# Kernel optimization log

Measured on AMD Instinct MI355X. Metric: run time of the kernel, lower is better.

Reference implementation:

```python
import jax, jax.numpy as jnp
import numpy as np

DIM = 2048
HQ = 32
HKV = 8
HEAD_DIM = DIM // HQ          # 64
GROUP = HQ // HKV             # 4 q-heads per kv-head
B, S = 2, 2048


def setup_inputs() -> dict:
    key = jax.random.key(0)
    ks = jax.random.split(key, 12)
    sc_in = 1.0 / np.sqrt(DIM)   # lecun_normal fan-in scaling
    inp = {
        "q": jax.random.normal(ks[0], (B, S, DIM), jnp.float32),
        "k": jax.random.normal(ks[1], (B, S, DIM), jnp.float32),
        "v": jax.random.normal(ks[2], (B, S, DIM), jnp.float32),
        # causal 0/1 mask: module computes scores -= 1/mask + 1, so 0 -> -inf (masked), 1 -> -2 (softmax-invariant shift)
        "mask": jnp.tril(jnp.ones((S, S), jnp.int32)),
        "Wq": jax.random.normal(ks[3], (DIM, HQ * HEAD_DIM), jnp.float32) * sc_in,
        "bq": jnp.zeros((HQ * HEAD_DIM,), jnp.float32),
        "Wk": jax.random.normal(ks[4], (DIM, HKV * HEAD_DIM), jnp.float32) * sc_in,
        "bk": jnp.zeros((HKV * HEAD_DIM,), jnp.float32),
        "Wv": jax.random.normal(ks[5], (DIM, HKV * HEAD_DIM), jnp.float32) * sc_in,
        "bv": jnp.zeros((HKV * HEAD_DIM,), jnp.float32),
        "Wo": jax.random.normal(ks[6], (DIM, DIM), jnp.float32) * (1.0 / np.sqrt(DIM)),
        "bo": jnp.zeros((DIM,), jnp.float32),
    }
    return inp


def reference(q, k, v, mask, Wq, bq, Wk, bk, Wv, bv, Wo, bo):
    b, s, _ = q.shape
    # projections -> per-head layout
    qx = (q @ Wq + bq).reshape(b, s, HKV, GROUP, HEAD_DIM)   # grouped q-heads
    kx = (k @ Wk + bk).reshape(b, s, HKV, HEAD_DIM)
    vx = (v @ Wv + bv).reshape(b, s, HKV, HEAD_DIM)
    # scores[b, h, g, i, j] = q_i . k_j ; same math as repeating kv heads GROUP times
    scores = jnp.einsum('bihgd,bjhd->bhgij', qx, kx) / jnp.sqrt(
        jnp.asarray(HEAD_DIM, qx.dtype))
    # module's masking: scores -= 1/mask + 1  (mask==0 -> -inf, mask==1 -> -2)
    scores = scores - (1.0 / mask.astype(scores.dtype) + 1.0)
    probs = jax.nn.softmax(scores, axis=-1)
    out = jnp.einsum('bhgij,bjhd->bihgd', probs, vx).reshape(b, s, DIM)
    out = out @ Wo + bo
    return out
```

## Files before the change

kernel.cpp:

```cpp
#include <hip/hip_runtime.h>

typedef unsigned short u16;
typedef unsigned int u32;
typedef __attribute__((ext_vector_type(8))) short short8v;
typedef __attribute__((ext_vector_type(4))) float f32x4;

#define DIM 2048
#define HQN 32
#define HKVN 8
#define HD 64
#define BB 2
#define SS 2048
#define MTOT (BB*SS)
#define NKV (HKVN*HD)

__device__ __forceinline__ u16 f2bf(float f){
  u32 u = __float_as_uint(f);
  u += 0x7FFFu + ((u >> 16) & 1u);
  return (u16)(u >> 16);
}

__device__ __forceinline__ u32 cvtpk(float a, float b){
  u32 r; asm("v_cvt_pk_bf16_f32 %0, %1, %2" : "=v"(r) : "v"(a), "v"(b)); return r;
}

__device__ __forceinline__ void gload_lds16(const void* g, void* l){
  __builtin_amdgcn_global_load_lds((const __attribute__((address_space(1))) u32*)g,
                                   (__attribute__((address_space(3))) u32*)l, 16, 0, 0);
}

#define WAITVM_(N) asm volatile("s_waitcnt vmcnt(" #N ")" ::: "memory")
#define WAITVM(N) WAITVM_(N)
#define CFENCE()  asm volatile("" ::: "memory")
#define BARF()    do { CFENCE(); __builtin_amdgcn_s_barrier(); CFENCE(); } while(0)
#define MF(a,b,cc) __builtin_amdgcn_mfma_f32_16x16x32_bf16((a),(b),(cc),0,0,0)

__global__ __launch_bounds__(256) void cast3_kernel(const float4* __restrict__ q,
                                                    const float4* __restrict__ k,
                                                    const float4* __restrict__ v,
                                                    u16* __restrict__ qo,
                                                    u16* __restrict__ ko,
                                                    u16* __restrict__ vo, int n4){
  const int z = blockIdx.y;
  const float4* in = z==0 ? q : (z==1 ? k : v);
  u16* out = z==0 ? qo : (z==1 ? ko : vo);
  int i = blockIdx.x*256 + threadIdx.x;
  if (i < n4){
    float4 f = in[i];
    union { u16 s[4]; unsigned long long u; } r;
    r.s[0]=f2bf(f.x); r.s[1]=f2bf(f.y); r.s[2]=f2bf(f.z); r.s[3]=f2bf(f.w);
    *(unsigned long long*)(out + (size_t)i*4) = r.u;
  }
}

__global__ __launch_bounds__(256) void transpose4_kernel(const float* __restrict__ Wq,
                                                         const float* __restrict__ Wk,
                                                         const float* __restrict__ Wv,
                                                         const float* __restrict__ Wo,
                                                         u16* __restrict__ WqT,
                                                         u16* __restrict__ WkT,
                                                         u16* __restrict__ WvT,
                                                         u16* __restrict__ WoT){
  const int z = blockIdx.z;
  const float* W = z==0?Wq:(z==1?Wk:(z==2?Wv:Wo));
  u16* WT = z==0?WqT:(z==1?WkT:(z==2?WvT:WoT));
  const int N = (z==1||z==2) ? NKV : DIM;
  const int K = DIM;
  int n0 = blockIdx.x*32, k0 = blockIdx.y*32;
  if (n0 >= N) return;
  __shared__ float tile[32][33];
  int tx = threadIdx.x & 31, ty = threadIdx.x >> 5;
  #pragma unroll
  for (int i=0;i<4;i++){
    int kk = ty + i*8;
    tile[kk][tx] = W[(size_t)(k0+kk)*N + n0 + tx];
  }
  __syncthreads();
  #pragma unroll
  for (int i=0;i<4;i++){
    int n = ty + i*8;
    WT[(size_t)(n0+n)*K + k0 + tx] = f2bf(tile[tx][n]);
  }
}

template<int MODE>
__global__ __launch_bounds__(512, 4) void gemm_pipe_kernel(
    const u16* __restrict__ Aq, const u16* __restrict__ Ak, const u16* __restrict__ Av,
    const u16* __restrict__ BT,
    const float* __restrict__ bq, const float* __restrict__ bk, const float* __restrict__ bv,
    u16* __restrict__ Qp, u16* __restrict__ Kp, u16* __restrict__ Vp,
    float* __restrict__ Cout)
{
  __shared__ __align__(16) u16 lds[3][12288];
  const int t = threadIdx.x, lane = t & 63, w = t >> 6;
  const int wm = w >> 1, wn = w & 1, g = lane >> 4, c = lane & 15;
  int bid = blockIdx.x;
  int seg, m0, n0;
  if (MODE == 0){
    bid = (bid & 7)*48 + (bid >> 3);
    if (bid < 256){ seg = 0; m0 = (bid >> 4)*256; n0 = (bid & 15)*128; }
    else { int u = bid - 256; seg = 1 + (u >> 6); int u6 = u & 63;
           m0 = (u6 >> 2)*256; n0 = (seg == 1 ? 2048 : 2560) + (u6 & 3)*128; }
  } else {
    bid = (bid & 7)*32 + (bid >> 3);
    seg = 0; m0 = (bid >> 4)*256; n0 = (bid & 15)*128;
  }
  const u16* A = (MODE==1 || seg==0) ? Aq : (seg==1 ? Ak : Av);
  const float* bias = (MODE==1 || seg==0) ? bq : (seg==1 ? bk : bv);
  const int nsegbase = (MODE==1 || seg==0) ? 0 : (seg==1 ? 2048 : 2560);

  const u16* gA0 = A  + (size_t)(m0 +       (t>>2))*DIM + (t&3)*8;
  const u16* gA1 = A  + (size_t)(m0 + 128 + (t>>2))*DIM + (t&3)*8;
  const u16* gB  = BT + (size_t)(n0 +       (t>>2))*DIM + (t&3)*8;

#define STG_A(KT, SL) do{ size_t ko_=(size_t)(KT)*32; \
    gload_lds16(gA0+ko_, &lds[SL][t*8]); \
    gload_lds16(gA1+ko_, &lds[SL][4096 + t*8]); }while(0)
#define STG_B(KT, SL) do{ \
    gload_lds16(gB + (size_t)(KT)*32, &lds[SL][8192 + t*8]); }while(0)

  const f32x4 fzero = {0.f,0.f,0.f,0.f};
  f32x4 acc[4][4];
  #pragma unroll
  for (int i=0;i<4;i++)
    #pragma unroll
    for (int j=0;j<4;j++) acc[i][j] = fzero;

  const int arow = wm*64 + c;
  const int brow = wn*64 + c;

#define TILE(SC, SG, KT, DOSTAGE, DOVM, VMN) do{                                \
    const u16* Ls_ = &lds[SC][0];                                               \
    short8v a0_ = *(const short8v*)&Ls_[(arow +  0)*32 + 8*g];                  \
    short8v a1_ = *(const short8v*)&Ls_[(arow + 16)*32 + 8*g];                  \
    short8v b0_ = *(const short8v*)&Ls_[8192 + (brow +  0)*32 + 8*g];           \
    short8v b1_ = *(const short8v*)&Ls_[8192 + (brow + 16)*32 + 8*g];           \
    short8v b2_ = *(const short8v*)&Ls_[8192 + (brow + 32)*32 + 8*g];           \
    short8v b3_ = *(const short8v*)&Ls_[8192 + (brow + 48)*32 + 8*g];           \
    if (DOSTAGE) STG_A((KT)+2, SG);                                             \
    BARF();                                                                     \
    __builtin_amdgcn_s_setprio(1);                                              \
    acc[0][0]=MF(a0_,b0_,acc[0][0]); acc[0][1]=MF(a0_,b1_,acc[0][1]);           \
    acc[0][2]=MF(a0_,b2_,acc[0][2]); acc[0][3]=MF(a0_,b3_,acc[0][3]);           \
    acc[1][0]=MF(a1_,b0_,acc[1][0]); acc[1][1]=MF(a1_,b1_,acc[1][1]);           \
    acc[1][2]=MF(a1_,b2_,acc[1][2]); acc[1][3]=MF(a1_,b3_,acc[1][3]);           \
    __builtin_amdgcn_s_setprio(0);                                              \
    BARF();                                                                     \
    short8v a2_ = *(const short8v*)&Ls_[(arow + 32)*32 + 8*g];                  \
    short8v a3_ = *(const short8v*)&Ls_[(arow + 48)*32 + 8*g];                  \
    if (DOSTAGE) STG_B((KT)+2, SG);                                             \
    BARF();                                                                     \
    __builtin_amdgcn_s_setprio(1);                                              \
    acc[2][0]=MF(a2_,b0_,acc[2][0]); acc[2][1]=MF(a2_,b1_,acc[2][1]);           \
    acc[2][2]=MF(a2_,b2_,acc[2][2]); acc[2][3]=MF(a2_,b3_,acc[2][3]);           \
    acc[3][0]=MF(a3_,b0_,acc[3][0]); acc[3][1]=MF(a3_,b1_,acc[3][1]);           \
    acc[3][2]=MF(a3_,b2_,acc[3][2]); acc[3][3]=MF(a3_,b3_,acc[3][3]);           \
    __builtin_amdgcn_s_setprio(0);                                              \
    if (DOVM) WAITVM(VMN);                                                      \
    BARF();                                                                     \
  }while(0)

  STG_A(0, 0); STG_B(0, 0);
  STG_A(1, 1); STG_B(1, 1);
  WAITVM(3);
  BARF();

  for (int tt = 0; tt < 62; ++tt){
    const int sc = tt % 3;
    const int sg = (tt + 2) % 3;
    TILE(sc, sg, tt, 1, 1, 3);
  }
  TILE(62 % 3, 0, 62, 0, 1, 0);
  TILE(63 % 3, 0, 63, 0, 0, 0);
#undef TILE
#undef STG_A
#undef STG_B

  __syncthreads();

  if (MODE == 1){
    #pragma unroll
    for (int fm=0; fm<4; fm++){
      #pragma unroll
      for (int fn=0; fn<4; fn++){
        int n = n0 + wn*64 + fn*16 + c;
        float bvv = bias[n];
        #pragma unroll
        for (int r=0; r<4; r++){
          int m = m0 + wm*64 + fm*16 + 4*g + r;
          Cout[(size_t)m*DIM + n] = acc[fm][fn][r] + bvv;
        }
      }
    }
  } else {
    u16* st = &lds[0][0] + w*4096;
    if (seg == 2){
      #pragma unroll
      for (int fm=0; fm<4; fm++){
        #pragma unroll
        for (int fn=0; fn<4; fn++){
          float bvv = bias[n0 - nsegbase + wn*64 + fn*16 + c];
          int vbase = (fm>>1)*2048 + fn*512 + (g*16 + c)*8 + (fm&1)*4;
          *(u32*)&st[vbase]     = cvtpk(acc[fm][fn][0]+bvv, acc[fm][fn][1]+bvv);
          *(u32*)&st[vbase + 2] = cvtpk(acc[fm][fn][2]+bvv, acc[fm][fn][3]+bvv);
        }
      }
    } else {
      #pragma unroll
      for (int fm=0; fm<4; fm++){
        #pragma unroll
        for (int fn=0; fn<4; fn++){
          float bvv = bias[n0 - nsegbase + wn*64 + fn*16 + c];
          int sbase = (fm>>1)*2048 + ((fm&1)*2 + (fn>>1))*512
                    + (c>>2)*128 + (fn&1)*4 + (c&3);
          #pragma unroll
          for (int r=0; r<4; r++)
            st[sbase + (4*g + r)*8] = f2bf(acc[fm][fn][r] + bvv);
        }
      }
    }
    __syncthreads();
    const int bb = m0 >> 11;
    const int st0 = ((m0 & 2047) >> 5) + wm*2;
    u16* dst;
    if (seg == 0)      dst = Qp + (((size_t)bb*HQN  + (n0>>6)        + wn) << 17);
    else if (seg == 1) dst = Kp + (((size_t)bb*HKVN + ((n0-2048)>>6) + wn) << 17);
    else               dst = Vp + (((size_t)bb*HKVN + ((n0-2560)>>6) + wn) << 17);
    dst += (size_t)st0*2048;
    #pragma unroll
    for (int i=0;i<8;i++)
      *(short8v*)(dst + lane*8 + i*512) = *(const short8v*)(st + lane*8 + i*512);
  }
}

__global__ __launch_bounds__(256) void attn_kernel(const u16* __restrict__ Qp,
                                                   const u16* __restrict__ Kp,
                                                   const u16* __restrict__ Vp,
                                                   u16* __restrict__ Aout){
  const int grp = blockIdx.x & 15;
  const int jj  = blockIdx.x >> 4;
  const int b   = grp >> 3;
  const int hkv = grp & 7;
  const int t = threadIdx.x;
  const int lane = t & 63, w = t >> 6;
  const int g = lane >> 4, c = lane & 15;
  const int hq = hkv*4 + w;

  __shared__ __align__(16) u16 Kt[2][2048];
  __shared__ __align__(16) u16 Vt[2][2048];

  const u16* Kb = Kp + (((size_t)b*HKVN + hkv) << 17);
  const u16* Vb = Vp + (((size_t)b*HKVN + hkv) << 17);
  const u16* Qb = Qp + (((size_t)b*HQN + hq) << 17);
  const float SCL = 0.18033688011112042f;
  const f32x4 fzero = {0.f,0.f,0.f,0.f};

  for (int half = 0; half < 2; ++half){
    const int T = half ? jj : (63 - jj);

    short8v qf[2][2];
    {
      const u16* qs = Qb + (size_t)T*2048 + lane*8;
      qf[0][0] = *(const short8v*)(qs);
      qf[0][1] = *(const short8v*)(qs + 512);
      qf[1][0] = *(const short8v*)(qs + 1024);
      qf[1][1] = *(const short8v*)(qs + 1536);
    }
    float l_r[2] = {0.f, 0.f};
    f32x4 o[2][4];
    #pragma unroll
    for (int qi=0; qi<2; qi++)
      #pragma unroll
      for (int f=0; f<4; f++) o[qi][f] = fzero;

    gload_lds16(Kb + t*8, &Kt[0][t*8]);
    gload_lds16(Vb + t*8, &Vt[0][t*8]);
    asm volatile("s_waitcnt vmcnt(0)" ::: "memory");
    __syncthreads();

    int cur = 0;
    for (int kt = 0; kt <= T; ++kt){
      if (kt < T){
        gload_lds16(Kb + (size_t)(kt+1)*2048 + t*8, &Kt[cur^1][t*8]);
        gload_lds16(Vb + (size_t)(kt+1)*2048 + t*8, &Vt[cur^1][t*8]);
      }
      short8v kf0 = *(const short8v*)&Kt[cur][lane*8];
      short8v kf1 = *(const short8v*)&Kt[cur][512 + lane*8];
      short8v kf2 = *(const short8v*)&Kt[cur][1024 + lane*8];
      short8v kf3 = *(const short8v*)&Kt[cur][1536 + lane*8];
      short8v vf0 = *(const short8v*)&Vt[cur][lane*8];
      short8v vf1 = *(const short8v*)&Vt[cur][512 + lane*8];
      short8v vf2 = *(const short8v*)&Vt[cur][1024 + lane*8];
      short8v vf3 = *(const short8v*)&Vt[cur][1536 + lane*8];
      const bool diag = (kt == T);
      #pragma unroll
      for (int qi=0; qi<2; qi++){
        f32x4 s0 = fzero, s1 = fzero;
        __builtin_amdgcn_s_setprio(1);
        s0 = MF(kf0, qf[qi][0], s0);
        s0 = MF(kf1, qf[qi][1], s0);
        s1 = MF(kf2, qf[qi][0], s1);
        s1 = MF(kf3, qf[qi][1], s1);
        __builtin_amdgcn_s_setprio(0);
        float p0[4], p1[4];
        #pragma unroll
        for (int r=0; r<4; r++){
          p0[r] = __builtin_amdgcn_exp2f(s0[r]*SCL);
          p1[r] = __builtin_amdgcn_exp2f(s1[r]*SCL);
        }
        if (diag){
          const int qloc = qi*16 + c;
          #pragma unroll
          for (int r=0; r<4; r++){
            if (4*g + r      > qloc) p0[r] = 0.f;
            if (16 + 4*g + r > qloc) p1[r] = 0.f;
          }
        }
        l_r[qi] += (p0[0]+p0[1]) + (p0[2]+p0[3]) + (p1[0]+p1[1]) + (p1[2]+p1[3]);
        union { u32 u[4]; short8v v; } pu;
        pu.u[0] = cvtpk(p0[0], p0[1]);
        pu.u[1] = cvtpk(p0[2], p0[3]);
        pu.u[2] = cvtpk(p1[0], p1[1]);
        pu.u[3] = cvtpk(p1[2], p1[3]);
        __builtin_amdgcn_s_setprio(1);
        o[qi][0] = MF(pu.v, vf0, o[qi][0]);
        o[qi][1] = MF(pu.v, vf1, o[qi][1]);
        o[qi][2] = MF(pu.v, vf2, o[qi][2]);
        o[qi][3] = MF(pu.v, vf3, o[qi][3]);
        __builtin_amdgcn_s_setprio(0);
      }
      asm volatile("s_waitcnt vmcnt(0)" ::: "memory");
      __syncthreads();
      cur ^= 1;
    }

    #pragma unroll
    for (int qi=0; qi<2; qi++){
      float ls = l_r[qi];
      ls += __shfl_xor(ls, 16);
      ls += __shfl_xor(ls, 32);
      float li = 1.0f / ls;
      float lf[4];
      #pragma unroll
      for (int r=0; r<4; r++) lf[r] = __shfl(li, 4*g + r);
      #pragma unroll
      for (int f=0; f<4; f++){
        #pragma unroll
        for (int r=0; r<4; r++){
          int q = T*32 + qi*16 + 4*g + r;
          Aout[((size_t)b*SS + q)*DIM + hq*HD + f*16 + c] = f2bf(o[qi][f][r]*lf[r]);
        }
      }
    }
  }
}

extern "C" void kernel_launch(void* const* d_in, const int* in_sizes, int n_in,
                              void* d_out, int out_size, void* d_ws, size_t ws_size,
                              hipStream_t stream){
  const float* q  = (const float*)d_in[0];
  const float* k  = (const float*)d_in[1];
  const float* v  = (const float*)d_in[2];
  const float* Wq = (const float*)d_in[4];
  const float* bq = (const float*)d_in[5];
  const float* Wk = (const float*)d_in[6];
  const float* bk = (const float*)d_in[7];
  const float* Wv = (const float*)d_in[8];
  const float* bv = (const float*)d_in[9];
  const float* Wo = (const float*)d_in[10];
  const float* bo = (const float*)d_in[11];
  float* out = (float*)d_out;

  char* ws = (char*)d_ws;
  u16* q_bf = (u16*)ws; ws += (size_t)MTOT*DIM*2;
  u16* k_bf = (u16*)ws; ws += (size_t)MTOT*DIM*2;
  u16* v_bf = (u16*)ws; ws += (size_t)MTOT*DIM*2;
  u16* WqT  = (u16*)ws; ws += (size_t)DIM*DIM*2;
  u16* WkT  = (u16*)ws; ws += (size_t)NKV*DIM*2;
  u16* WvT  = (u16*)ws; ws += (size_t)NKV*DIM*2;
  u16* WoT  = (u16*)ws; ws += (size_t)DIM*DIM*2;
  u16* Qp   = (u16*)ws; ws += (size_t)MTOT*DIM*2;
  u16* Kp   = (u16*)ws; ws += (size_t)MTOT*NKV*2;
  u16* Vp   = (u16*)ws; ws += (size_t)MTOT*NKV*2;
  u16* attn = (u16*)ws; ws += (size_t)MTOT*DIM*2;

  const int n4 = MTOT*DIM/4;
  cast3_kernel<<<dim3(n4/256, 3), 256, 0, stream>>>((const float4*)q, (const float4*)k,
                                                    (const float4*)v, q_bf, k_bf, v_bf, n4);
  transpose4_kernel<<<dim3(DIM/32, DIM/32, 4), 256, 0, stream>>>(Wq, Wk, Wv, Wo,
                                                                 WqT, WkT, WvT, WoT);
  gemm_pipe_kernel<0><<<384, 512, 0, stream>>>(q_bf, k_bf, v_bf, WqT,
                                               bq, bk, bv, Qp, Kp, Vp, nullptr);
  attn_kernel<<<512, 256, 0, stream>>>(Qp, Kp, Vp, attn);
  gemm_pipe_kernel<1><<<256, 512, 0, stream>>>(attn, nullptr, nullptr, WoT,
                                               bo, nullptr, nullptr,
                                               nullptr, nullptr, nullptr, out);
}
```

Before: 216.3 us.

## Split GEMM into larger-tile QKV and O kernels with swizzled double-buffered LDS

Replaces the shared templated GEMM with two specialised kernels. The QKV projection moves to 256x256 tiles (192 blocks, 8x4 accumulators per warp), and the output GEMM keeps 256x128 tiles but uses a 2x4 warp grid. Both now use K=64 steps with XOR-swizzled LDS and a double-buffered, four-phase load/compute schedule. The aim is more data reuse per byte loaded and fewer LDS bank conflicts. The cost is much more LDS and more registers per block, which lowers occupancy (launch bounds drop to 2 blocks per CU), and the QKV launch has fewer blocks than the machine has CUs, which can hurt wave balance.

```diff
diff --git a/kernel.cpp b/kernel.cpp
--- a/kernel.cpp
+++ b/kernel.cpp
@@ -83,154 +83,265 @@
   }
 }
 
-template<int MODE>
-__global__ __launch_bounds__(512, 4) void gemm_pipe_kernel(
-    const u16* __restrict__ Aq, const u16* __restrict__ Ak, const u16* __restrict__ Av,
-    const u16* __restrict__ BT,
-    const float* __restrict__ bq, const float* __restrict__ bk, const float* __restrict__ bv,
-    u16* __restrict__ Qp, u16* __restrict__ Kp, u16* __restrict__ Vp,
-    float* __restrict__ Cout)
-{
-  __shared__ __align__(16) u16 lds[3][12288];
+__global__ __launch_bounds__(512, 2) void gemm_qkv_kernel(const u16* __restrict__ Aq,
+                                                          const u16* __restrict__ Ak,
+                                                          const u16* __restrict__ Av,
+                                                          const u16* __restrict__ BT,
+                                                          const float* __restrict__ bq,
+                                                          const float* __restrict__ bk,
+                                                          const float* __restrict__ bv,
+                                                          u16* __restrict__ Qp,
+                                                          u16* __restrict__ Kp,
+                                                          u16* __restrict__ Vp){
+  __shared__ __align__(16) u16 lds[65536];
+  char* ldsb = (char*)lds;
   const int t = threadIdx.x, lane = t & 63, w = t >> 6;
-  const int wm = w >> 1, wn = w & 1, g = lane >> 4, c = lane & 15;
+  const int wm = w >> 2, wn = w & 3, g = lane >> 4, c = lane & 15;
   int bid = blockIdx.x;
-  int seg, m0, n0;
-  if (MODE == 0){
-    bid = (bid & 7)*48 + (bid >> 3);
-    if (bid < 256){ seg = 0; m0 = (bid >> 4)*256; n0 = (bid & 15)*128; }
-    else { int u = bid - 256; seg = 1 + (u >> 6); int u6 = u & 63;
-           m0 = (u6 >> 2)*256; n0 = (seg == 1 ? 2048 : 2560) + (u6 & 3)*128; }
-  } else {
-    bid = (bid & 7)*32 + (bid >> 3);
-    seg = 0; m0 = (bid >> 4)*256; n0 = (bid & 15)*128;
-  }
-  const u16* A = (MODE==1 || seg==0) ? Aq : (seg==1 ? Ak : Av);
-  const float* bias = (MODE==1 || seg==0) ? bq : (seg==1 ? bk : bv);
-  const int nsegbase = (MODE==1 || seg==0) ? 0 : (seg==1 ? 2048 : 2560);
-
-  const u16* gA0 = A  + (size_t)(m0 +       (t>>2))*DIM + (t&3)*8;
-  const u16* gA1 = A  + (size_t)(m0 + 128 + (t>>2))*DIM + (t&3)*8;
-  const u16* gB  = BT + (size_t)(n0 +       (t>>2))*DIM + (t&3)*8;
-
-#define STG_A(KT, SL) do{ size_t ko_=(size_t)(KT)*32; \
-    gload_lds16(gA0+ko_, &lds[SL][t*8]); \
-    gload_lds16(gA1+ko_, &lds[SL][4096 + t*8]); }while(0)
-#define STG_B(KT, SL) do{ \
-    gload_lds16(gB + (size_t)(KT)*32, &lds[SL][8192 + t*8]); }while(0)
+  bid = (bid & 7)*24 + (bid >> 3);
+  const int mt = bid / 12, nt = bid - mt*12;
+  const int m0 = mt*256, n0 = nt*256;
+  const int seg = (n0 >= 2560) ? 2 : (n0 >= 2048 ? 1 : 0);
+  const u16* A = seg==0 ? Aq : (seg==1 ? Ak : Av);
+  const float* bias = seg==0 ? bq : (seg==1 ? bk : bv);
+  const int nbase = seg==0 ? 0 : (seg==1 ? 2048 : 2560);
+
+  const int rA = t >> 3;
+  const int kc = ((t & 7) ^ (rA & 7)) * 8;
+  const u16* gA = A  + (size_t)(m0 + rA)*DIM + kc;
+  const u16* gB = BT + (size_t)(n0 + ((rA>>5)<<6) + (rA & 31))*DIM + kc;
+
+  const u32 ko0 = (u32)((g*16) ^ ((c&7)<<4));
+  const u32 ko1 = (u32)((64 + g*16) ^ ((c&7)<<4));
+  const u32 aoff = wm*8192 + c*128;
+  const u32 boff = wn*4096 + c*128;
+
+#define STGA_(PA, KT, ABASE) do{ \
+    gload_lds16(gA + (size_t)(KT)*64 + (size_t)((PA)*64)*DIM,       ldsb + (ABASE) + (PA)*16384 + t*16); \
+    gload_lds16(gA + (size_t)(KT)*64 + (size_t)((PA)*64+128)*DIM,   ldsb + (ABASE) + (PA)*16384 + 8192 + t*16); }while(0)
+#define STGB_(PB, KT, BBASE) do{ \
+    gload_lds16(gB + (size_t)(KT)*64 + (size_t)((PB)*32)*DIM,       ldsb + (BBASE) + (PB)*16384 + t*16); \
+    gload_lds16(gB + (size_t)(KT)*64 + (size_t)((PB)*32+128)*DIM,   ldsb + (BBASE) + (PB)*16384 + 8192 + t*16); }while(0)
+#define LD8(OFF) (*(const short8v*)(ldsb + (OFF)))
 
   const f32x4 fzero = {0.f,0.f,0.f,0.f};
-  f32x4 acc[4][4];
+  f32x4 acc[8][4];
   #pragma unroll
-  for (int i=0;i<4;i++)
+  for (int i=0;i<8;i++)
     #pragma unroll
     for (int j=0;j<4;j++) acc[i][j] = fzero;
 
-  const int arow = wm*64 + c;
-  const int brow = wn*64 + c;
-
-#define TILE(SC, SG, KT, DOSTAGE, DOVM, VMN) do{                                \
-    const u16* Ls_ = &lds[SC][0];                                               \
-    short8v a0_ = *(const short8v*)&Ls_[(arow +  0)*32 + 8*g];                  \
-    short8v a1_ = *(const short8v*)&Ls_[(arow + 16)*32 + 8*g];                  \
-    short8v b0_ = *(const short8v*)&Ls_[8192 + (brow +  0)*32 + 8*g];           \
-    short8v b1_ = *(const short8v*)&Ls_[8192 + (brow + 16)*32 + 8*g];           \
-    short8v b2_ = *(const short8v*)&Ls_[8192 + (brow + 32)*32 + 8*g];           \
-    short8v b3_ = *(const short8v*)&Ls_[8192 + (brow + 48)*32 + 8*g];           \
-    if (DOSTAGE) STG_A((KT)+2, SG);                                             \
-    BARF();                                                                     \
-    __builtin_amdgcn_s_setprio(1);                                              \
-    acc[0][0]=MF(a0_,b0_,acc[0][0]); acc[0][1]=MF(a0_,b1_,acc[0][1]);           \
-    acc[0][2]=MF(a0_,b2_,acc[0][2]); acc[0][3]=MF(a0_,b3_,acc[0][3]);           \
-    acc[1][0]=MF(a1_,b0_,acc[1][0]); acc[1][1]=MF(a1_,b1_,acc[1][1]);           \
-    acc[1][2]=MF(a1_,b2_,acc[1][2]); acc[1][3]=MF(a1_,b3_,acc[1][3]);           \
-    __builtin_amdgcn_s_setprio(0);                                              \
-    BARF();                                                                     \
-    short8v a2_ = *(const short8v*)&Ls_[(arow + 32)*32 + 8*g];                  \
-    short8v a3_ = *(const short8v*)&Ls_[(arow + 48)*32 + 8*g];                  \
-    if (DOSTAGE) STG_B((KT)+2, SG);                                             \
-    BARF();                                                                     \
-    __builtin_amdgcn_s_setprio(1);                                              \
-    acc[2][0]=MF(a2_,b0_,acc[2][0]); acc[2][1]=MF(a2_,b1_,acc[2][1]);           \
-    acc[2][2]=MF(a2_,b2_,acc[2][2]); acc[2][3]=MF(a2_,b3_,acc[2][3]);           \
-    acc[3][0]=MF(a3_,b0_,acc[3][0]); acc[3][1]=MF(a3_,b1_,acc[3][1]);           \
-    acc[3][2]=MF(a3_,b2_,acc[3][2]); acc[3][3]=MF(a3_,b3_,acc[3][3]);           \
-    __builtin_amdgcn_s_setprio(0);                                              \
-    if (DOVM) WAITVM(VMN);                                                      \
-    BARF();                                                                     \
+#define MM16(FM0, FN0) do{ __builtin_amdgcn_s_setprio(1); \
+    _Pragma("unroll") for (int q=0;q<4;q++) \
+      _Pragma("unroll") for (int s=0;s<2;s++){ \
+        acc[(FM0)+q][(FN0)+s] = MF(a_[q][0], b_[s][0], acc[(FM0)+q][(FN0)+s]); \
+        acc[(FM0)+q][(FN0)+s] = MF(a_[q][1], b_[s][1], acc[(FM0)+q][(FN0)+s]); } \
+    __builtin_amdgcn_s_setprio(0); }while(0)
+
+#define RD_A(PABASE) do{ _Pragma("unroll") for (int q=0;q<4;q++){ \
+    a_[q][0] = LD8((PABASE) + aoff + q*2048 + ko0); \
+    a_[q][1] = LD8((PABASE) + aoff + q*2048 + ko1); } }while(0)
+#define RD_B(PBBASE) do{ _Pragma("unroll") for (int q=0;q<2;q++){ \
+    b_[q][0] = LD8((PBBASE) + boff + q*2048 + ko0); \
+    b_[q][1] = LD8((PBBASE) + boff + q*2048 + ko1); } }while(0)
+
+#define QSTEP(TT, CUR, DOSTG, TAIL) do{ \
+    const u32 AC = (CUR)*32768,  BC = 65536 + (CUR)*32768; \
+    const u32 AN = (CUR^1)*32768, BN = 65536 + (CUR^1)*32768; \
+    short8v a_[4][2], b_[2][2]; \
+    RD_A(AC); RD_B(BC); \
+    if (DOSTG) STGA_(0, (TT)+1, AN); \
+    BARF(); \
+    MM16(0,0); \
+    if (TAIL) { WAITVM(2); } else { WAITVM(4); } \
+    BARF(); \
+    RD_B(BC + 16384); \
+    if (DOSTG) STGB_(0, (TT)+1, BN); \
+    BARF(); \
+    MM16(0,2); \
+    if (TAIL) { WAITVM(0); } else { WAITVM(4); } \
+    BARF(); \
+    RD_A(AC + 16384); \
+    if (DOSTG) STGB_(1, (TT)+1, BN); \
+    BARF(); \
+    MM16(4,2); \
+    BARF(); \
+    RD_B(BC); \
+    if (DOSTG) STGA_(1, (TT)+1, AN); \
+    BARF(); \
+    MM16(4,0); \
+    if (!TAIL) { WAITVM(4); } \
+    BARF(); \
   }while(0)
 
-  STG_A(0, 0); STG_B(0, 0);
-  STG_A(1, 1); STG_B(1, 1);
-  WAITVM(3);
+  STGA_(0, 0, 0); STGB_(0, 0, 65536); STGB_(1, 0, 65536); STGA_(1, 0, 0);
+  WAITVM(0);
   BARF();
 
-  for (int tt = 0; tt < 62; ++tt){
-    const int sc = tt % 3;
-    const int sg = (tt + 2) % 3;
-    TILE(sc, sg, tt, 1, 1, 3);
-  }
-  TILE(62 % 3, 0, 62, 0, 1, 0);
-  TILE(63 % 3, 0, 63, 0, 0, 0);
-#undef TILE
-#undef STG_A
-#undef STG_B
-
+  #pragma unroll 1
+  for (int tt = 0; tt < 30; tt += 2){
+    QSTEP(tt,   0, 1, 0);
+    QSTEP(tt+1, 1, 1, 0);
+  }
+  QSTEP(30, 0, 1, 0);
+  QSTEP(31, 1, 0, 1);
+#undef QSTEP
+
+  WAITVM(0);
   __syncthreads();
 
-  if (MODE == 1){
-    #pragma unroll
-    for (int fm=0; fm<4; fm++){
+  u16* st = lds + w*8192;
+  if (seg == 2){
+    #pragma unroll
+    for (int fm=0; fm<8; fm++){
       #pragma unroll
       for (int fn=0; fn<4; fn++){
-        int n = n0 + wn*64 + fn*16 + c;
-        float bvv = bias[n];
-        #pragma unroll
-        for (int r=0; r<4; r++){
-          int m = m0 + wm*64 + fm*16 + 4*g + r;
-          Cout[(size_t)m*DIM + n] = acc[fm][fn][r] + bvv;
-        }
+        float bvv = bias[n0 - nbase + wn*64 + fn*16 + c];
+        int vbase = (fm>>1)*2048 + fn*512 + (g*16 + c)*8 + (fm&1)*4;
+        *(u32*)&st[vbase]     = cvtpk(acc[fm][fn][0]+bvv, acc[fm][fn][1]+bvv);
+        *(u32*)&st[vbase + 2] = cvtpk(acc[fm][fn][2]+bvv, acc[fm][fn][3]+bvv);
       }
     }
   } else {
-    u16* st = &lds[0][0] + w*4096;
-    if (seg == 2){
-      #pragma unroll
-      for (int fm=0; fm<4; fm++){
+    #pragma unroll
+    for (int fm=0; fm<8; fm++){
+      #pragma unroll
+      for (int fn=0; fn<4; fn++){
+        float bvv = bias[n0 - nbase + wn*64 + fn*16 + c];
+        int sbase = (fm>>1)*2048 + ((fm&1)*2 + (fn>>1))*512 + (c>>2)*128 + (fn&1)*4 + (c&3);
         #pragma unroll
-        for (int fn=0; fn<4; fn++){
-          float bvv = bias[n0 - nsegbase + wn*64 + fn*16 + c];
-          int vbase = (fm>>1)*2048 + fn*512 + (g*16 + c)*8 + (fm&1)*4;
-          *(u32*)&st[vbase]     = cvtpk(acc[fm][fn][0]+bvv, acc[fm][fn][1]+bvv);
-          *(u32*)&st[vbase + 2] = cvtpk(acc[fm][fn][2]+bvv, acc[fm][fn][3]+bvv);
-        }
-      }
-    } else {
-      #pragma unroll
-      for (int fm=0; fm<4; fm++){
-        #pragma unroll
-        for (int fn=0; fn<4; fn++){
-          float bvv = bias[n0 - nsegbase + wn*64 + fn*16 + c];
-          int sbase = (fm>>1)*2048 + ((fm&1)*2 + (fn>>1))*512
-                    + (c>>2)*128 + (fn&1)*4 + (c&3);
-          #pragma unroll
-          for (int r=0; r<4; r++)
-            st[sbase + (4*g + r)*8] = f2bf(acc[fm][fn][r] + bvv);
-        }
+        for (int r=0; r<4; r++)
+          st[sbase + (4*g + r)*8] = f2bf(acc[fm][fn][r] + bvv);
       }
     }
-    __syncthreads();
+  }
+  __syncthreads();
+  {
     const int bb = m0 >> 11;
-    const int st0 = ((m0 & 2047) >> 5) + wm*2;
+    const int st0 = ((m0 & 2047) >> 5) + wm*4;
     u16* dst;
     if (seg == 0)      dst = Qp + (((size_t)bb*HQN  + (n0>>6)        + wn) << 17);
     else if (seg == 1) dst = Kp + (((size_t)bb*HKVN + ((n0-2048)>>6) + wn) << 17);
     else               dst = Vp + (((size_t)bb*HKVN + ((n0-2560)>>6) + wn) << 17);
     dst += (size_t)st0*2048;
     #pragma unroll
-    for (int i=0;i<8;i++)
+    for (int i=0;i<16;i++)
       *(short8v*)(dst + lane*8 + i*512) = *(const short8v*)(st + lane*8 + i*512);
   }
+#undef STGA_
+#undef STGB_
+#undef RD_A
+#undef RD_B
+#undef MM16
+}
+
+__global__ __launch_bounds__(512, 2) void gemm_o_kernel(const u16* __restrict__ A,
+                                                        const u16* __restrict__ BT,
+                                                        const float* __restrict__ bias,
+                                                        float* __restrict__ C){
+  __shared__ __align__(16) u16 lds[49152];
+  char* ldsb = (char*)lds;
+  const int t = threadIdx.x, lane = t & 63, w = t >> 6;
+  const int wm = w >> 2, wn = w & 3, g = lane >> 4, c = lane & 15;
+  int bid = blockIdx.x;
+  bid = (bid & 7)*32 + (bid >> 3);
+  const int m0 = (bid >> 4)*256, n0 = (bid & 15)*128;
+
+  const int rA = t >> 3;
+  const int kc = ((t & 7) ^ (rA & 7)) * 8;
+  const u16* gA = A  + (size_t)(m0 + rA)*DIM + kc;
+  const u16* gB = BT + (size_t)(n0 + ((rA>>4)<<5) + (rA & 15))*DIM + kc;
+
+  const u32 ko0 = (u32)((g*16) ^ ((c&7)<<4));
+  const u32 ko1 = (u32)((64 + g*16) ^ ((c&7)<<4));
+  const u32 aoff = wm*8192 + c*128;
+  const u32 boffo = wn*2048 + c*128;
+
+#define STGA_(PA, KT, ABASE) do{ \
+    gload_lds16(gA + (size_t)(KT)*64 + (size_t)((PA)*64)*DIM,       ldsb + (ABASE) + (PA)*16384 + t*16); \
+    gload_lds16(gA + (size_t)(KT)*64 + (size_t)((PA)*64+128)*DIM,   ldsb + (ABASE) + (PA)*16384 + 8192 + t*16); }while(0)
+#define STGB_(PB, KT, BBASE) do{ \
+    gload_lds16(gB + (size_t)(KT)*64 + (size_t)((PB)*16)*DIM,       ldsb + (BBASE) + (PB)*8192 + t*16); }while(0)
+#define LD8(OFF) (*(const short8v*)(ldsb + (OFF)))
+
+  const f32x4 fzero = {0.f,0.f,0.f,0.f};
+  f32x4 acc[8][2];
+  #pragma unroll
+  for (int i=0;i<8;i++){ acc[i][0] = fzero; acc[i][1] = fzero; }
+
+#define MMO(FM0, FN) do{ __builtin_amdgcn_s_setprio(1); \
+    _Pragma("unroll") for (int q=0;q<4;q++){ \
+      acc[(FM0)+q][FN] = MF(a_[q][0], b_[0], acc[(FM0)+q][FN]); \
+      acc[(FM0)+q][FN] = MF(a_[q][1], b_[1], acc[(FM0)+q][FN]); } \
+    __builtin_amdgcn_s_setprio(0); }while(0)
+
+#define RD_A(PABASE) do{ _Pragma("unroll") for (int q=0;q<4;q++){ \
+    a_[q][0] = LD8((PABASE) + aoff + q*2048 + ko0); \
+    a_[q][1] = LD8((PABASE) + aoff + q*2048 + ko1); } }while(0)
+#define RD_B(PBBASE) do{ \
+    b_[0] = LD8((PBBASE) + boffo + ko0); \
+    b_[1] = LD8((PBBASE) + boffo + ko1); }while(0)
+
+#define OSTEP(TT, CUR, DOSTG, TAIL) do{ \
+    const u32 AC = (CUR)*32768,  BC = 65536 + (CUR)*16384; \
+    const u32 AN = (CUR^1)*32768, BN = 65536 + (CUR^1)*16384; \
+    short8v a_[4][2], b_[2]; \
+    RD_A(AC); RD_B(BC); \
+    if (DOSTG) STGA_(0, (TT)+1, AN); \
+    BARF(); \
+    MMO(0,0); \
+    if (TAIL) { WAITVM(2); } else { WAITVM(4); } \
+    BARF(); \
+    RD_B(BC + 8192); \
+    if (DOSTG) STGB_(0, (TT)+1, BN); \
+    BARF(); \
+    MMO(0,1); \
+    if (TAIL) { WAITVM(0); } else { WAITVM(3); } \
+    BARF(); \
+    RD_A(AC + 16384); \
+    if (DOSTG) STGB_(1, (TT)+1, BN); \
+    BARF(); \
+    MMO(4,1); \
+    BARF(); \
+    RD_B(BC); \
+    if (DOSTG) STGA_(1, (TT)+1, AN); \
+    BARF(); \
+    MMO(4,0); \
+    if (!TAIL) { WAITVM(3); } \
+    BARF(); \
+  }while(0)
+
+  STGA_(0, 0, 0); STGB_(0, 0, 65536); STGB_(1, 0, 65536); STGA_(1, 0, 0);
+  WAITVM(0);
+  BARF();
+
+  #pragma unroll 1
+  for (int tt = 0; tt < 30; tt += 2){
+    OSTEP(tt,   0, 1, 0);
+    OSTEP(tt+1, 1, 1, 0);
+  }
+  OSTEP(30, 0, 1, 0);
+  OSTEP(31, 1, 0, 1);
+#undef OSTEP
+
+  #pragma unroll
+  for (int fm=0; fm<8; fm++){
+    #pragma unroll
+    for (int fn=0; fn<2; fn++){
+      int n = n0 + wn*32 + fn*16 + c;
+      float bvv = bias[n];
+      #pragma unroll
+      for (int r=0; r<4; r++){
+        int m = m0 + wm*128 + fm*16 + 4*g + r;
+        C[(size_t)m*DIM + n] = acc[fm][fn][r] + bvv;
+      }
+    }
+  }
+#undef STGA_
+#undef STGB_
+#undef RD_A
+#undef RD_B
+#undef MMO
 }
 
 __global__ __launch_bounds__(256) void attn_kernel(const u16* __restrict__ Qp,
@@ -389,10 +500,8 @@
                                                     (const float4*)v, q_bf, k_bf, v_bf, n4);
   transpose4_kernel<<<dim3(DIM/32, DIM/32, 4), 256, 0, stream>>>(Wq, Wk, Wv, Wo,
                                                                  WqT, WkT, WvT, WoT);
-  gemm_pipe_kernel<0><<<384, 512, 0, stream>>>(q_bf, k_bf, v_bf, WqT,
-                                               bq, bk, bv, Qp, Kp, Vp, nullptr);
+  gemm_qkv_kernel<<<192, 512, 0, stream>>>(q_bf, k_bf, v_bf, WqT,
+                                           bq, bk, bv, Qp, Kp, Vp);
   attn_kernel<<<512, 256, 0, stream>>>(Qp, Kp, Vp, attn);
-  gemm_pipe_kernel<1><<<256, 512, 0, stream>>>(attn, nullptr, nullptr, WoT,
-                                               bo, nullptr, nullptr,
-                                               nullptr, nullptr, nullptr, out);
-}
+  gemm_o_kernel<<<256, 512, 0, stream>>>(attn, WoT, bo, out);
+}
```

New measurement: 198.8 us. 1.09x faster.
